# Kernel optimization log

Hardware: AMD Instinct MI355X
Metric: run time of the kernel (lower is better)

Reference implementation:

```python
import jax, jax.numpy as jnp
import numpy as np

B, CIN, COUT, T = 64, 2048, 2048, 128
BLOCK = 8            # structured-sparsity block size from _create_structured_sparse_mask
SPARSITY = 0.9       # keep probability per block = 1 - SPARSITY
SPIKE_PROB = 0.1     # binary input spike rate


def setup_inputs() -> dict:
    key = jax.random.key(0)
    k1, k2, k3 = jax.random.split(key, 3)
    # binary input spikes [B, Cin, T] (torch casts to int8; values are 0/1)
    spikes = (jax.random.uniform(k1, (B, CIN, T)) < SPIKE_PROB).astype(jnp.float32)
    # int8 quantized weights held as float32 (values in [-127,127))
    weights = jax.random.randint(k2, (COUT, CIN), -127, 127).astype(jnp.float32)
    # block-structured sparse connectivity mask, block 8x8, keep prob 0.1
    keep = jax.random.uniform(k3, (COUT // BLOCK, CIN // BLOCK)) > SPARSITY
    mask = jnp.repeat(jnp.repeat(keep, BLOCK, axis=0), BLOCK, axis=1).astype(jnp.float32)
    scale_exp = jnp.zeros((COUT,), dtype=jnp.int32)  # weight_scale_exp init zeros
    return {"spikes": spikes, "weights": weights, "mask": mask,
            "scale_exp": scale_exp, "threshold_exp": 7}


def reference(spikes, weights, mask, scale_exp, threshold_exp):
    # spikes: [B, Cin, T]; weights/mask: [Cout, Cin]; scale_exp: [Cout]
    masked_w = weights * mask                              # [Cout, Cin]
    scale = jnp.exp2(scale_exp.astype(jnp.float32))        # 2**weight_scale_exp per channel
    thr = jnp.float32(2.0) ** threshold_exp                # 2**threshold_exp (=128)
    s_t = jnp.transpose(spikes, (2, 0, 1))                 # [T, B, Cin]
    acc0 = jnp.zeros((spikes.shape[0], weights.shape[0]), jnp.float32)

    def step(acc, st):
        # integrate: sparse-masked matmul + power-of-two per-channel scale
        acc = acc + (st @ masked_w.T) * scale              # [B, Cout]
        spk = (acc >= thr).astype(jnp.float32)             # fire
        acc = acc * (1.0 - spk)                            # reset fired neurons to 0
        return acc, spk

    _, out = jax.lax.scan(step, acc0, s_t)                 # out: [T, B, Cout]
    return jnp.transpose(out, (1, 2, 0))                   # [B, Cout, T]
```

## Files before the change

### kernel.cpp

```cpp
#include <hip/hip_runtime.h>

#define BB   64
#define CIN  2048
#define COUT 2048
#define TT   128

#define NPAIR 64
#define NWIN  4
#define SLOTW 32

typedef int i32x4 __attribute__((ext_vector_type(4)));

__device__ __forceinline__ void async16(char* lds_dst, const char* g_src) {
    __builtin_amdgcn_global_load_lds(
        (const __attribute__((address_space(1))) void*)g_src,
        (__attribute__((address_space(3))) void*)lds_dst,
        16, 0, 0);
}

__global__ void prep1(const float* __restrict__ spikes,
                      const float* __restrict__ msk,
                      char* __restrict__ A,
                      unsigned long long* __restrict__ kb) {
    int bid = blockIdx.x;
    int tid = threadIdx.x;

    if (bid >= 2048) {
        int rb = bid - 2048;
        bool keep = (msk[(size_t)(rb * 8) * CIN + tid * 8] != 0.f);
        unsigned long long m = __ballot(keep);
        if ((tid & 63) == 0) kb[rb * 4 + (tid >> 6)] = m;
        return;
    }

    __shared__ float tile[32][256];
    int cg = bid & 7, tg = (bid >> 3) & 3, b = bid >> 5;
    int c0 = cg * 256, t0 = tg * 32;

    {
        const float* src = spikes + ((size_t)b * CIN + c0 + tid) * TT + t0;
#pragma unroll
        for (int j = 0; j < 8; ++j) {
            float4 v = *(const float4*)(src + j * 4);
            tile[j * 4 + 0][tid] = v.x;
            tile[j * 4 + 1][tid] = v.y;
            tile[j * 4 + 2][tid] = v.z;
            tile[j * 4 + 3][tid] = v.w;
        }
    }
    __syncthreads();

    const int cq = tid & 63, tw = tid >> 6;
#pragma unroll
    for (int s2 = 0; s2 < 8; ++s2) {
        int t = s2 * 4 + tw;
        float4 v = *(const float4*)&tile[t][cq * 4];
        unsigned pk = (v.x != 0.f ? 0x1u : 0u) | (v.y != 0.f ? 0x100u : 0u) |
                      (v.z != 0.f ? 0x10000u : 0u) | (v.w != 0.f ? 0x1000000u : 0u);
        *(unsigned*)(A + ((size_t)(b * TT) + t0 + t) * CIN + c0 + cq * 4) = pk;
    }
}

__global__ void prep2(const float* __restrict__ w,
                      const float* __restrict__ msk,
                      const unsigned long long* __restrict__ kb,
                      char* __restrict__ Bc,
                      unsigned short* __restrict__ lst,
                      unsigned* __restrict__ ofs_g,
                      unsigned* __restrict__ nch_g) {
    __shared__ unsigned sbm[256];
    __shared__ unsigned snch[256];
    __shared__ unsigned sofs[256];
    const int tid = threadIdx.x;
    const int pw_self = blockIdx.x;

    {
        int p = tid >> 2, wdw = tid & 3;
        unsigned long long r = kb[(4 * p + 0) * 4 + wdw] | kb[(4 * p + 1) * 4 + wdw] |
                               kb[(4 * p + 2) * 4 + wdw] | kb[(4 * p + 3) * 4 + wdw];
        unsigned long long t2 = r | (r >> 1);
        unsigned bm = 0u;
#pragma unroll
        for (int s = 0; s < 32; ++s)
            bm |= (unsigned)((t2 >> (2 * s)) & 1ull) << s;
        sbm[tid]  = bm;
        snch[tid] = (unsigned)((__popc(bm) + 3) >> 2);
    }
    __syncthreads();
    if (tid == 0) {
        unsigned run = 0;
#pragma unroll 4
        for (int i = 0; i < 256; ++i) { sofs[i] = run; run += snch[i] * 4; }
        ofs_g[pw_self] = sofs[pw_self];
        nch_g[pw_self] = snch[pw_self];
    }
    __syncthreads();

    const int p = pw_self >> 2, wdw = pw_self & 3;
    unsigned rem = sbm[pw_self];
    const unsigned o = sofs[pw_self];
    const unsigned nslots = snch[pw_self] * 4;

    for (unsigned j = 0; j < nslots; ++j) {
        int kl = 0;
        bool real = false;
        if (rem) { kl = __ffs(rem) - 1; rem &= rem - 1u; real = true; }
        int kk = wdw * SLOTW + kl;
        if (tid < 128) {
            int col = tid >> 2, q = tid & 3;
            unsigned pk = 0u;
            if (real) {
                size_t base = (size_t)(p * 32 + col) * CIN + kk * 16 + q * 4;
                float4 a = *(const float4*)(w + base);
                float4 m = *(const float4*)(msk + base);
                int b0 = (int)(char)(int)(a.x * m.x);
                int b1 = (int)(char)(int)(a.y * m.y);
                int b2 = (int)(char)(int)(a.z * m.z);
                int b3 = (int)(char)(int)(a.w * m.w);
                pk = (unsigned)((b0 & 0xFF) | ((b1 & 0xFF) << 8) | ((b2 & 0xFF) << 16) | (b3 << 24));
            }
            *(unsigned*)(Bc + (size_t)(o + j) * 512 + col * 16 + q * 4) = pk;
        }
        if (tid == 0) lst[o + j] = (unsigned short)(real ? kl : 0);
    }
}

__global__ void __launch_bounds__(512, 4)
snn_gemm_scan(const char* __restrict__ A,
              const char* __restrict__ Bc,
              const unsigned short* __restrict__ lst,
              const unsigned* __restrict__ ofs,
              const unsigned* __restrict__ nchv,
              const int* __restrict__ scale_exp,
              const int* __restrict__ thr_exp,
              float* __restrict__ out) {
    __shared__ __align__(16) union {
        char a[128 * 512];
        float c[128 * 132];
    } lds;
    __shared__ unsigned short slist[8][NWIN][SLOTW];
    __shared__ unsigned smeta_ofs[32];
    __shared__ unsigned smeta_nch[32];
    __shared__ unsigned pb[128 * 4];

    const int tid  = threadIdx.x;
    const int lane = tid & 63;
    const int w    = tid >> 6;
    const int wr   = w >> 2;
    const int wp   = w & 3;

    const int bid = blockIdx.x;
    const int b  = bid & 63;
    const int nt = bid >> 6;
    const int m0 = b * TT;
    const int p0 = nt * 8;

    const int mrow = lane & 15, kc = lane >> 4;

    if (tid < 64) {
        int i = tid & 31;
        unsigned g = (p0 + (i >> 2)) * 4 + (i & 3);
        if (tid < 32) smeta_ofs[i] = ofs[g];
        else          smeta_nch[i] = nchv[g];
    }
    {
        int pl = tid >> 6;
        int rest = tid & 63;
        int w2 = rest >> 4, e = (rest & 15) * 2;
        unsigned g = (p0 + pl) * 4 + w2;
        unsigned o = ofs[g];
        *(unsigned*)&slist[pl][w2][e] = *(const unsigned*)(lst + o + e);
    }

    i32x4 acc[4][2][2] = {};

    for (int wdw = 0; wdw < NWIN; ++wdw) {
        __syncthreads();
#pragma unroll
        for (int i = 0; i < 8; ++i) {
            int f = i * 512 + tid;
            int row = f >> 5, g0 = f & 31;
            int src = (g0 & ~7) | ((g0 & 7) ^ (row & 7));
            async16((char*)lds.a + (size_t)f * 16,
                    A + (size_t)(m0 + row) * CIN + wdw * 512 + src * 16);
        }
        __syncthreads();

#pragma unroll
        for (int pi = 0; pi < 2; ++pi) {
            const int pl = wp * 2 + pi;
            const unsigned o   = smeta_ofs[pl * 4 + wdw];
            const unsigned nch = smeta_nch[pl * 4 + wdw];
            const unsigned short* Lp = &slist[pl][wdw][0];
            if (nch == 0) continue;
            const char* bbase = Bc + (size_t)o * 512 + mrow * 16 + (size_t)kc * 512;

            int   kkN = (int)Lp[kc];
            i32x4 b0N = *(const i32x4*)bbase;
            for (unsigned c = 0; c < nch; ++c) {
                const int   kkC = kkN;
                const i32x4 b0C = b0N;
                i32x4 b1C = *(const i32x4*)(bbase + (size_t)c * 2048 + 256);
                if (c + 1 < nch) {
                    kkN = (int)Lp[(c + 1) * 4 + kc];
                    b0N = *(const i32x4*)(bbase + (size_t)(c + 1) * 2048);
                }
#pragma unroll
                for (int mf = 0; mf < 4; ++mf) {
                    int row = wr * 64 + mf * 16 + mrow;
                    i32x4 av = *(const i32x4*)((const char*)lds.a +
                                  row * 512 + ((kkC ^ (row & 7)) << 4));
                    acc[mf][pi][0] = __builtin_amdgcn_mfma_i32_16x16x64_i8(
                        av, b0C, acc[mf][pi][0], 0, 0, 0);
                }
#pragma unroll
                for (int mf = 0; mf < 4; ++mf) {
                    int row = wr * 64 + mf * 16 + mrow;
                    i32x4 av = *(const i32x4*)((const char*)lds.a +
                                  row * 512 + ((kkC ^ (row & 7)) << 4));
                    acc[mf][pi][1] = __builtin_amdgcn_mfma_i32_16x16x64_i8(
                        av, b1C, acc[mf][pi][1], 0, 0, 0);
                }
            }
        }
    }

    const float thr = exp2f((float)thr_exp[0]);
#pragma unroll
    for (int P = 0; P < 2; ++P) {
        __syncthreads();
        if ((wp >> 1) == P) {
            const int rb = (lane >> 4) * 4;
            const int cb = lane & 15;
            const int cbase = (wp & 1) * 64;
#pragma unroll
            for (int mf = 0; mf < 4; ++mf)
#pragma unroll
                for (int pi = 0; pi < 2; ++pi)
#pragma unroll
                    for (int cf = 0; cf < 2; ++cf)
#pragma unroll
                        for (int r = 0; r < 4; ++r)
                            lds.c[(wr * 64 + mf * 16 + rb + r) * 132 +
                                  cbase + pi * 32 + cf * 16 + cb] =
                                (float)acc[mf][pi][cf][r];
        }
        __syncthreads();

        if (tid < 128) {
            const float scale = exp2f((float)scale_exp[nt * 256 + P * 128 + tid]);
            float a = 0.f;
#pragma unroll
            for (int q = 0; q < 4; ++q) {
                unsigned bq = 0u;
#pragma unroll 8
                for (int j = 0; j < 32; ++j) {
                    a += lds.c[(q * 32 + j) * 132 + tid] * scale;
                    unsigned sp = (a >= thr) ? 1u : 0u;
                    if (sp) a = 0.f;
                    bq |= sp << j;
                }
                pb[tid * 4 + q] = bq;
            }
        }
        __syncthreads();

        const int t4 = tid & 31, u = tid >> 5;
#pragma unroll
        for (int s2 = 0; s2 < 8; ++s2) {
            int co = s2 * 16 + u;
            unsigned wb  = pb[co * 4 + (t4 >> 3)];
            unsigned nib = (wb >> ((t4 & 7) * 4)) & 0xFu;
            float4 v;
            v.x = (float)(nib & 1u);
            v.y = (float)((nib >> 1) & 1u);
            v.z = (float)((nib >> 2) & 1u);
            v.w = (float)((nib >> 3) & 1u);
            *(float4*)(out + (size_t)(b * COUT + nt * 256 + P * 128 + co) * TT
                       + t4 * 4) = v;
        }
    }
}

extern "C" void kernel_launch(void* const* d_in, const int* in_sizes, int n_in,
                              void* d_out, int out_size, void* d_ws, size_t ws_size,
                              hipStream_t stream) {
    const float* spikes  = (const float*)d_in[0];
    const float* weights = (const float*)d_in[1];
    const float* mask    = (const float*)d_in[2];
    const int*   scale_e = (const int*)d_in[3];
    const int*   thr_e   = (const int*)d_in[4];
    float* out = (float*)d_out;

    char* ws = (char*)d_ws;
    char*               Ai8  = ws;
    char*               Bc   = ws + 16777216;
    unsigned short*     lstp = (unsigned short*)(ws + 20709376);
    unsigned*           ofsp = (unsigned*)(ws + 20725760);
    unsigned*           nchp = (unsigned*)(ws + 20726784);
    unsigned long long* kbp  = (unsigned long long*)(ws + 20727808);

    prep1<<<2048 + 256, 256, 0, stream>>>(spikes, mask, Ai8, kbp);
    prep2<<<NPAIR * NWIN, 256, 0, stream>>>(weights, mask, kbp, Bc, lstp, ofsp, nchp);
    snn_gemm_scan<<<8 * BB, 512, 0, stream>>>(Ai8, Bc, lstp, ofsp, nchp,
                                              scale_e, thr_e, out);
}
```

Baseline: 222.1 us.

## Double-buffer A windows in LDS and give each wave one full pair

The GEMM-scan kernel now double-buffers the activation windows in LDS, prefetching window k+2 while computing window k, with explicit vmcnt waits and barriers in place of full syncthreads. Each wave now owns one column pair across all 128 rows instead of half the rows for two pairs, which gives every wave a uniform chunk count and lets it load all A fragments before issuing the MFMAs. Doubling LDS lowers the launch bound to 2 blocks per CU. prep2 also moves slot-list generation into a single thread and spreads the B packing across all 256 threads, two slots per iteration.

Result: faster. 209.2 us (-5.8%).

```diff
diff --git a/kernel.cpp b/kernel.cpp
--- a/kernel.cpp
+++ b/kernel.cpp
@@ -68,9 +68,10 @@
                       unsigned short* __restrict__ lst,
                       unsigned* __restrict__ ofs_g,
                       unsigned* __restrict__ nch_g) {
-    __shared__ unsigned sbm[256];
     __shared__ unsigned snch[256];
     __shared__ unsigned sofs[256];
+    __shared__ unsigned sbm_self;
+    __shared__ short skl[SLOTW];
     const int tid = threadIdx.x;
     const int pw_self = blockIdx.x;
 
@@ -83,7 +84,7 @@
 #pragma unroll
         for (int s = 0; s < 32; ++s)
             bm |= (unsigned)((t2 >> (2 * s)) & 1ull) << s;
-        sbm[tid]  = bm;
+        if (tid == pw_self) sbm_self = bm;
         snch[tid] = (unsigned)((__popc(bm) + 3) >> 2);
     }
     __syncthreads();
@@ -93,23 +94,31 @@
         for (int i = 0; i < 256; ++i) { sofs[i] = run; run += snch[i] * 4; }
         ofs_g[pw_self] = sofs[pw_self];
         nch_g[pw_self] = snch[pw_self];
+        unsigned rem = sbm_self;
+        unsigned ns = snch[pw_self] * 4;
+        unsigned o0 = sofs[pw_self];
+        for (unsigned j = 0; j < ns; ++j) {
+            int kl = -1;
+            if (rem) { kl = __ffs(rem) - 1; rem &= rem - 1u; }
+            skl[j] = (short)kl;
+            lst[o0 + j] = (unsigned short)(kl >= 0 ? kl : 0);
+        }
     }
     __syncthreads();
 
     const int p = pw_self >> 2, wdw = pw_self & 3;
-    unsigned rem = sbm[pw_self];
     const unsigned o = sofs[pw_self];
     const unsigned nslots = snch[pw_self] * 4;
 
-    for (unsigned j = 0; j < nslots; ++j) {
-        int kl = 0;
-        bool real = false;
-        if (rem) { kl = __ffs(rem) - 1; rem &= rem - 1u; real = true; }
-        int kk = wdw * SLOTW + kl;
-        if (tid < 128) {
-            int col = tid >> 2, q = tid & 3;
+    const int col = (tid & 127) >> 2, q = tid & 3;
+    const unsigned jo = tid >> 7;
+    for (unsigned j0 = 0; j0 < nslots; j0 += 2) {
+        unsigned j = j0 + jo;
+        if (j < nslots) {
+            int kl = skl[j];
             unsigned pk = 0u;
-            if (real) {
+            if (kl >= 0) {
+                int kk = wdw * SLOTW + kl;
                 size_t base = (size_t)(p * 32 + col) * CIN + kk * 16 + q * 4;
                 float4 a = *(const float4*)(w + base);
                 float4 m = *(const float4*)(msk + base);
@@ -121,11 +130,10 @@
             }
             *(unsigned*)(Bc + (size_t)(o + j) * 512 + col * 16 + q * 4) = pk;
         }
-        if (tid == 0) lst[o + j] = (unsigned short)(real ? kl : 0);
-    }
-}
-
-__global__ void __launch_bounds__(512, 4)
+    }
+}
+
+__global__ void __launch_bounds__(512, 2)
 snn_gemm_scan(const char* __restrict__ A,
               const char* __restrict__ Bc,
               const unsigned short* __restrict__ lst,
@@ -135,7 +143,7 @@
               const int* __restrict__ thr_exp,
               float* __restrict__ out) {
     __shared__ __align__(16) union {
-        char a[128 * 512];
+        char a[2][128 * 512];
         float c[128 * 132];
     } lds;
     __shared__ unsigned short slist[8][NWIN][SLOTW];
@@ -146,8 +154,6 @@
     const int tid  = threadIdx.x;
     const int lane = tid & 63;
     const int w    = tid >> 6;
-    const int wr   = w >> 2;
-    const int wp   = w & 3;
 
     const int bid = blockIdx.x;
     const int b  = bid & 63;
@@ -172,78 +178,87 @@
         *(unsigned*)&slist[pl][w2][e] = *(const unsigned*)(lst + o + e);
     }
 
-    i32x4 acc[4][2][2] = {};
-
-    for (int wdw = 0; wdw < NWIN; ++wdw) {
-        __syncthreads();
+    i32x4 acc[8][2] = {};
+
+    auto stage = [&](int wdw, int buf) {
 #pragma unroll
         for (int i = 0; i < 8; ++i) {
             int f = i * 512 + tid;
             int row = f >> 5, g0 = f & 31;
             int src = (g0 & ~7) | ((g0 & 7) ^ (row & 7));
-            async16((char*)lds.a + (size_t)f * 16,
+            async16((char*)lds.a[buf] + (size_t)f * 16,
                     A + (size_t)(m0 + row) * CIN + wdw * 512 + src * 16);
         }
-        __syncthreads();
-
-#pragma unroll
-        for (int pi = 0; pi < 2; ++pi) {
-            const int pl = wp * 2 + pi;
-            const unsigned o   = smeta_ofs[pl * 4 + wdw];
-            const unsigned nch = smeta_nch[pl * 4 + wdw];
-            const unsigned short* Lp = &slist[pl][wdw][0];
-            if (nch == 0) continue;
-            const char* bbase = Bc + (size_t)o * 512 + mrow * 16 + (size_t)kc * 512;
-
+    };
+
+    stage(0, 0);
+    stage(1, 1);
+    asm volatile("s_waitcnt vmcnt(8) lgkmcnt(0)" ::: "memory");
+    __builtin_amdgcn_s_barrier();
+
+#pragma unroll
+    for (int wdw = 0; wdw < NWIN; ++wdw) {
+        const char* sa = (const char*)lds.a[wdw & 1];
+        const unsigned o   = smeta_ofs[w * 4 + wdw];
+        const unsigned nch = smeta_nch[w * 4 + wdw];
+        const unsigned short* Lp = &slist[w][wdw][0];
+        const char* bbase = Bc + (size_t)o * 512 + mrow * 16 + (size_t)kc * 512;
+
+        if (nch) {
             int   kkN = (int)Lp[kc];
             i32x4 b0N = *(const i32x4*)bbase;
+            i32x4 b1N = *(const i32x4*)(bbase + 256);
             for (unsigned c = 0; c < nch; ++c) {
                 const int   kkC = kkN;
-                const i32x4 b0C = b0N;
-                i32x4 b1C = *(const i32x4*)(bbase + (size_t)c * 2048 + 256);
+                const i32x4 b0C = b0N, b1C = b1N;
                 if (c + 1 < nch) {
                     kkN = (int)Lp[(c + 1) * 4 + kc];
                     b0N = *(const i32x4*)(bbase + (size_t)(c + 1) * 2048);
+                    b1N = *(const i32x4*)(bbase + (size_t)(c + 1) * 2048 + 256);
                 }
-#pragma unroll
-                for (int mf = 0; mf < 4; ++mf) {
-                    int row = wr * 64 + mf * 16 + mrow;
-                    i32x4 av = *(const i32x4*)((const char*)lds.a +
-                                  row * 512 + ((kkC ^ (row & 7)) << 4));
-                    acc[mf][pi][0] = __builtin_amdgcn_mfma_i32_16x16x64_i8(
-                        av, b0C, acc[mf][pi][0], 0, 0, 0);
-                }
-#pragma unroll
-                for (int mf = 0; mf < 4; ++mf) {
-                    int row = wr * 64 + mf * 16 + mrow;
-                    i32x4 av = *(const i32x4*)((const char*)lds.a +
-                                  row * 512 + ((kkC ^ (row & 7)) << 4));
-                    acc[mf][pi][1] = __builtin_amdgcn_mfma_i32_16x16x64_i8(
-                        av, b1C, acc[mf][pi][1], 0, 0, 0);
+                const int swz = mrow * 512 + ((kkC ^ (mrow & 7)) << 4);
+                i32x4 av[8];
+#pragma unroll
+                for (int mf = 0; mf < 8; ++mf)
+                    av[mf] = *(const i32x4*)(sa + mf * 8192 + swz);
+#pragma unroll
+                for (int mf = 0; mf < 8; ++mf) {
+                    acc[mf][0] = __builtin_amdgcn_mfma_i32_16x16x64_i8(
+                        av[mf], b0C, acc[mf][0], 0, 0, 0);
+                    acc[mf][1] = __builtin_amdgcn_mfma_i32_16x16x64_i8(
+                        av[mf], b1C, acc[mf][1], 0, 0, 0);
                 }
             }
         }
+
+        __builtin_amdgcn_s_barrier();
+        if (wdw + 1 < NWIN) {
+            if (wdw + 2 < NWIN) {
+                stage(wdw + 2, wdw & 1);
+                asm volatile("s_waitcnt vmcnt(8)" ::: "memory");
+            } else {
+                asm volatile("s_waitcnt vmcnt(0)" ::: "memory");
+            }
+            __builtin_amdgcn_s_barrier();
+        }
     }
 
     const float thr = exp2f((float)thr_exp[0]);
 #pragma unroll
     for (int P = 0; P < 2; ++P) {
         __syncthreads();
-        if ((wp >> 1) == P) {
+        if ((w >> 2) == P) {
             const int rb = (lane >> 4) * 4;
             const int cb = lane & 15;
-            const int cbase = (wp & 1) * 64;
-#pragma unroll
-            for (int mf = 0; mf < 4; ++mf)
-#pragma unroll
-                for (int pi = 0; pi < 2; ++pi)
-#pragma unroll
-                    for (int cf = 0; cf < 2; ++cf)
-#pragma unroll
-                        for (int r = 0; r < 4; ++r)
-                            lds.c[(wr * 64 + mf * 16 + rb + r) * 132 +
-                                  cbase + pi * 32 + cf * 16 + cb] =
-                                (float)acc[mf][pi][cf][r];
+            const int cbase = (w & 3) * 32;
+#pragma unroll
+            for (int mf = 0; mf < 8; ++mf)
+#pragma unroll
+                for (int cf = 0; cf < 2; ++cf)
+#pragma unroll
+                    for (int r = 0; r < 4; ++r)
+                        lds.c[(mf * 16 + rb + r) * 132 + cbase + cf * 16 + cb] =
+                            (float)acc[mf][cf][r];
         }
         __syncthreads();
 
```
